# Optimization experiments

Measured on AMD Instinct MI355X. Metric: run time of the kernel, lower is better.

## Reference

```python
import jax, jax.numpy as jnp
import numpy as np

APP_DIM = 27
FEA_PE = 6
VIEW_PE = 6
FEATURE_C = 128
DENSITY_SHIFT = -10.0
DISTANCE_SCALE = 25.0
IN_MLPC = 2 * VIEW_PE * 3 + 2 * FEA_PE * APP_DIM + 3 + APP_DIM  # 390


def positional_encoding(x, freqs):
    # x: [..., C] -> [..., 2*freqs*C]
    freq_bands = (2.0 ** jnp.arange(freqs)).astype(x.dtype)
    pts = (x[..., None] * freq_bands).reshape(x.shape[:-1] + (freqs * x.shape[-1],))
    return jnp.concatenate([jnp.sin(pts), jnp.cos(pts)], axis=-1)


def alpha2weights(alpha):
    # alpha: [N_rays, N_samples]; last sample forced opaque (as in source)
    alpha = alpha.at[:, -1].set(1.0)
    trans = jnp.concatenate(
        [jnp.ones((alpha.shape[0], 1), alpha.dtype), 1.0 - alpha + 1e-10], axis=-1)
    T = jnp.cumprod(trans, axis=-1)
    weights = alpha * T[:, :-1]
    return weights, T


def setup_inputs() -> dict:
    key = jax.random.key(0)
    ks = jax.random.split(key, 12)
    N_rays, N_samples = 4096, 128
    sigma_feat = jax.random.normal(ks[0], (N_rays, N_samples), jnp.float32)
    app_features = 0.1 * jax.random.normal(ks[1], (N_rays, N_samples, APP_DIM), jnp.float32)
    vd = jax.random.normal(ks[2], (N_rays, N_samples, 3), jnp.float32)
    viewdirs = vd / (jnp.linalg.norm(vd, axis=-1, keepdims=True) + 1e-8)
    dists = 0.02 * jax.random.uniform(ks[3], (N_rays, N_samples), jnp.float32)

    def linear(k, fan_in, fan_out):
        kw, kb = jax.random.split(k)
        lim = 1.0 / np.sqrt(fan_in)
        W = jax.random.uniform(kw, (fan_in, fan_out), jnp.float32, -lim, lim)
        b = jax.random.uniform(kb, (fan_out,), jnp.float32, -lim, lim)
        return W, b

    W1, b1 = linear(ks[4], IN_MLPC, FEATURE_C)
    W2, b2 = linear(ks[5], FEATURE_C, FEATURE_C)
    W3, _ = linear(ks[6], FEATURE_C, 3)
    b3 = jnp.zeros((3,), jnp.float32)  # bias of last layer initialized to 0 in source
    return {"sigma_feat": sigma_feat, "app_features": app_features,
            "viewdirs": viewdirs, "dists": dists,
            "W1": W1, "b1": b1, "W2": W2, "b2": b2, "W3": W3, "b3": b3}


def reference(sigma_feat, app_features, viewdirs, dists, W1, b1, W2, b2, W3, b3):
    # feature2density: softplus with density_shift
    sigma = jax.nn.softplus(sigma_feat + DENSITY_SHIFT)
    alpha = 1.0 - jnp.exp(-sigma * dists * DISTANCE_SCALE)  # [N_rays, N_samples]
    weights, _T = alpha2weights(alpha)

    # MLPRender_Fea: cat[features, viewdirs, PE(features), PE(viewdirs)]
    mlp_in = jnp.concatenate(
        [app_features, viewdirs,
         positional_encoding(app_features, FEA_PE),
         positional_encoding(viewdirs, VIEW_PE)], axis=-1)  # [R, S, 390]
    h = jax.nn.relu(jnp.einsum('rsc,cf->rsf', mlp_in, W1) + b1)
    h = jax.nn.relu(jnp.einsum('rsf,fg->rsg', h, W2) + b2)
    rgb = jax.nn.sigmoid(jnp.einsum('rsg,go->rso', h, W3) + b3)  # [R, S, 3]

    rgb_map = jnp.sum(weights[..., None] * rgb, axis=-2)  # [R, 3]
    return rgb_map
```

## Files before the change

### kernel.cpp

```cpp
#include <hip/hip_runtime.h>
#include <math.h>

typedef unsigned short u16;
using bf16x8 = __attribute__((ext_vector_type(8))) short;
using f32x4  = __attribute__((ext_vector_type(4))) float;

#define NS      128
#define NBLOCKS 4096
#define KS1     15
#define NSLICE  19

#define POOLSZ 16384

#define BAR() do { asm volatile("s_waitcnt lgkmcnt(0)" ::: "memory");        \
                   __builtin_amdgcn_s_barrier();                              \
                   asm volatile("" ::: "memory"); } while (0)

#define MF(A,B,C) __builtin_amdgcn_mfma_f32_16x16x32_bf16((A),(B),(C),0,0,0)

__device__ __forceinline__ u16 f2bf(float f) {
    unsigned int i = __float_as_uint(f);
    return (u16)((i + 0x7FFFu + ((i >> 16) & 1u)) >> 16);
}

__device__ __forceinline__ unsigned pk(float hi, float lo) {
    unsigned r;
    asm("v_cvt_pk_bf16_f32 %0, %1, %2" : "=v"(r) : "v"(lo), "v"(hi));
    return r;
}
__device__ __forceinline__ u16 f2bf1(float f) {
    return (u16)((__float_as_uint(f) + 0x8000u) >> 16);
}

__device__ __forceinline__ int afoff_h(int m, int k) {
    int chunk = ((k >> 5) * 8 + (m >> 4)) * 64 + ((k >> 3) & 3) * 16 + (m & 15);
    chunk ^= (k >> 3) & 3;
    return chunk * 8 + (k & 7);
}

__device__ __forceinline__ int orig_k(int ch, int slot) {
    if (ch < 27) {
        if (slot == 0) return ch;
        if (slot <= 6) return 30 + ch * 6 + (slot - 1);
        return 192 + ch * 6 + (slot - 7);
    } else {
        int c = ch - 27;
        if (slot == 0) return 27 + c;
        if (slot <= 6) return 354 + c * 6 + (slot - 1);
        return 372 + c * 6 + (slot - 7);
    }
}

__device__ __forceinline__ float ldch(const float* ap, const float* vp, int c) {
    return (c < 27) ? ap[c] : vp[c - 27];
}

__device__ __forceinline__ void build_x(u16* Xb, int m_b, int cl_b, float v) {
    float rev = v * 0.15915494309189535f;
    rev -= floorf(rev);
    float s0 = __builtin_amdgcn_sinf(rev);
    float c0 = __builtin_amdgcn_cosf(rev);
    float s1 = 2.f * s0 * c0, c1 = c0 * c0 - s0 * s0;
    float s2 = 2.f * s1 * c1, c2 = c1 * c1 - s1 * s1;
    float s3 = 2.f * s2 * c2, c3 = c2 * c2 - s2 * s2;
    float s4 = 2.f * s3 * c3, c4 = c3 * c3 - s3 * s3;
    float s5 = 2.f * s4 * c4, c5 = c4 * c4 - s4 * s4;
    uint4 lo, hi;
    lo.x = pk(s0, v);  lo.y = pk(s2, s1);  lo.z = pk(s4, s3);  lo.w = pk(c0, s5);
    hi.x = pk(c2, c1); hi.y = pk(c4, c3);  hi.z = pk(0.f, c5); hi.w = 0u;
    int base = (m_b >> 4) * 512 + ((2 * cl_b) * 16 + (m_b & 15)) * 8;
    *(uint4*)(Xb + base)       = lo;
    *(uint4*)(Xb + base + 128) = hi;
}

__global__ __launch_bounds__(256) void prep_kernel(
    const float* __restrict__ W1, const float* __restrict__ W2,
    const float* __restrict__ W3, u16* __restrict__ ws)
{
    int idx = blockIdx.x * 256 + threadIdx.x;
    if (idx < 61440) {
        int j = idx & 7, lane = (idx >> 3) & 63, nt = (idx >> 9) & 7, ks = idx >> 12;
        int q = lane >> 4, l15 = lane & 15;
        int klocal = q * 8 + j;
        int ch = ks * 2 + (klocal >> 4);
        int slot = klocal & 15;
        int n = nt * 16 + l15;
        ws[idx] = (slot < 13) ? f2bf(W1[orig_k(ch, slot) * 128 + n]) : (u16)0;
    } else if (idx < 77824) {
        int i2 = idx - 61440;
        int j = i2 & 7, lane = (i2 >> 3) & 63, nt = (i2 >> 9) & 7, ks = i2 >> 12;
        int k = ks * 32 + (lane >> 4) * 8 + j;
        int n = nt * 16 + (lane & 15);
        ws[idx] = f2bf(W2[k * 128 + n]);
    } else if (idx < 79872) {
        int i3 = idx - 77824;
        int j = i3 & 7, lane = (i3 >> 3) & 63, ks = i3 >> 9;
        int k = ks * 32 + (lane >> 4) * 8 + j;
        int n = lane & 15;
        ws[idx] = (n < 3) ? f2bf(W3[k * 3 + n]) : (u16)0;
    }
}

#define LOADB(N0,N1,N2,N3, s)                                                 \
    if ((s) < NSLICE) {                                                       \
        const u16* wp = wp0 + (s) * 4096;                                     \
        N0 = *(const bf16x8*)(wp);                                            \
        N1 = *(const bf16x8*)(wp + 512);                                      \
        N2 = *(const bf16x8*)(wp + 1024);                                     \
        N3 = *(const bf16x8*)(wp + 1536);                                     \
    }

#define BODYX(s, C0,C1,C2,C3, N0,N1,N2,N3)                                    \
  {                                                                           \
    LOADB(N0,N1,N2,N3, (s)+2);                                                \
    const u16* ab = pool + ((((s)>>1)&1) ? 8192 : 0) + (((s)&1)*4096)         \
                    + (wm*128 + lane)*8;                                      \
    bf16x8 a0 = *(const bf16x8*)(ab);                                         \
    bf16x8 a1 = *(const bf16x8*)(ab + 512);                                   \
    __builtin_amdgcn_s_setprio(1);                                            \
    acc[0][0]=MF(a0,C0,acc[0][0]); acc[0][1]=MF(a0,C1,acc[0][1]);             \
    acc[0][2]=MF(a0,C2,acc[0][2]); acc[0][3]=MF(a0,C3,acc[0][3]);             \
    acc[1][0]=MF(a1,C0,acc[1][0]); acc[1][1]=MF(a1,C1,acc[1][1]);             \
    acc[1][2]=MF(a1,C2,acc[1][2]); acc[1][3]=MF(a1,C3,acc[1][3]);             \
    __builtin_amdgcn_s_setprio(0);                                            \
  }

#define BODYH(s, C0,C1,C2,C3, N0,N1,N2,N3)                                    \
  {                                                                           \
    LOADB(N0,N1,N2,N3, (s)+2);                                                \
    int cb0 = ((((s)-15)*512) + wm*128 + lane) ^ quad;                        \
    bf16x8 a0 = *(const bf16x8*)(pool + cb0*8);                               \
    bf16x8 a1 = *(const bf16x8*)(pool + (cb0+64)*8);                          \
    __builtin_amdgcn_s_setprio(1);                                            \
    acc[0][0]=MF(a0,C0,acc[0][0]); acc[0][1]=MF(a0,C1,acc[0][1]);             \
    acc[0][2]=MF(a0,C2,acc[0][2]); acc[0][3]=MF(a0,C3,acc[0][3]);             \
    acc[1][0]=MF(a1,C0,acc[1][0]); acc[1][1]=MF(a1,C1,acc[1][1]);             \
    acc[1][2]=MF(a1,C2,acc[1][2]); acc[1][3]=MF(a1,C3,acc[1][3]);             \
    __builtin_amdgcn_s_setprio(0);                                            \
  }

#define GEND(g)                                                               \
  {                                                                           \
    if (4*((g)+3) + cl < 30) pv_nxt2 = ldch(ap, vp, 4*((g)+3) + cl);          \
    if (4*((g)+1) + cl < 30)                                                  \
        build_x(pool + ((((g)+1)&1) ? 8192 : 0) + (cl>>1)*4096, row, cl&1,    \
                pv_cur);                                                      \
    pv_cur = pv_nxt; pv_nxt = pv_nxt2;                                        \
    BAR();                                                                    \
  }

__global__ __launch_bounds__(512, 4) void render_kernel(
    const float* __restrict__ sigma_g, const float* __restrict__ app_g,
    const float* __restrict__ view_g,  const float* __restrict__ dists_g,
    const float* __restrict__ b1_g,    const float* __restrict__ b2_g,
    const float* __restrict__ b3_g,    const u16* __restrict__ ws,
    float* __restrict__ out_g)
{
    __shared__ __align__(16) u16 pool[POOLSZ];
    __shared__ __align__(16) float part[NS * 3];
    __shared__ float scanS;
    __shared__ float sum2[6];

    const int tid  = threadIdx.x;
    const int lane = tid & 63;
    const int wave = tid >> 6;
    const int l15  = lane & 15;
    const int quad = lane >> 4;
    const int wm   = wave >> 1;
    const int wn   = wave & 1;

    const int r  = blockIdx.x;
    const int rb = r * NS;
    const int row = tid & 127;
    const int cl  = tid >> 7;
    const float* ap = app_g  + (rb + row) * 27;
    const float* vp = view_g + (rb + row) * 3;

    const u16* wp0 = ws + wn * 2048 + lane * 8;
    bf16x8 bP0, bP1, bP2, bP3, bQ0, bQ1, bQ2, bQ3, bR0, bR1, bR2, bR3;
    LOADB(bP0, bP1, bP2, bP3, 0);
    LOADB(bQ0, bQ1, bQ2, bQ3, 1);

    float b1r[4];
    #pragma unroll
    for (int nt = 0; nt < 4; ++nt) b1r[nt] = b1_g[wn * 64 + nt * 16 + l15];

    float pv_cur  = ldch(ap, vp, cl);
    float pv_nxt  = ldch(ap, vp, 4 + cl);
    float pv_nxt2 = ldch(ap, vp, 8 + cl);

    float alpha = 0.f, prod = 1.f, wr = 0.f;
    if (tid < NS) {
        float x  = sigma_g[rb + tid] - 10.f;
        float sp = (x > 20.f) ? x : log1pf(expf(x));
        alpha = 1.f - expf(-sp * dists_g[rb + tid] * 25.f);
        if (tid == NS - 1) alpha = 1.f;
        float tb = 1.f - alpha + 1e-10f;
        prod = tb;
        #pragma unroll
        for (int d = 1; d < 64; d <<= 1) {
            float v = __shfl_up(prod, d);
            if (lane >= d) prod *= v;
        }
        if (tid == 63) scanS = prod;
    }

    build_x(pool + (cl >> 1) * 4096, row, cl & 1, pv_cur);
    pv_cur = pv_nxt; pv_nxt = pv_nxt2;
    BAR();

    if (tid < NS) {
        float prev = __shfl_up(prod, 1);
        float base = (lane == 0) ? 1.f : prev;
        float scale = (wave == 1) ? scanS : 1.f;
        wr = alpha * base * scale;
    }

    const f32x4 vzero = {0.f, 0.f, 0.f, 0.f};
    f32x4 acc[2][4];
    #pragma unroll
    for (int mt = 0; mt < 2; ++mt)
        #pragma unroll
        for (int nt = 0; nt < 4; ++nt) acc[mt][nt] = vzero;

    BODYX(0,  bP0,bP1,bP2,bP3, bR0,bR1,bR2,bR3);
    BODYX(1,  bQ0,bQ1,bQ2,bQ3, bP0,bP1,bP2,bP3);  GEND(0);
    BODYX(2,  bR0,bR1,bR2,bR3, bQ0,bQ1,bQ2,bQ3);
    BODYX(3,  bP0,bP1,bP2,bP3, bR0,bR1,bR2,bR3);  GEND(1);
    BODYX(4,  bQ0,bQ1,bQ2,bQ3, bP0,bP1,bP2,bP3);
    BODYX(5,  bR0,bR1,bR2,bR3, bQ0,bQ1,bQ2,bQ3);  GEND(2);
    BODYX(6,  bP0,bP1,bP2,bP3, bR0,bR1,bR2,bR3);
    BODYX(7,  bQ0,bQ1,bQ2,bQ3, bP0,bP1,bP2,bP3);  GEND(3);
    BODYX(8,  bR0,bR1,bR2,bR3, bQ0,bQ1,bQ2,bQ3);
    BODYX(9,  bP0,bP1,bP2,bP3, bR0,bR1,bR2,bR3);  GEND(4);
    BODYX(10, bQ0,bQ1,bQ2,bQ3, bP0,bP1,bP2,bP3);
    BODYX(11, bR0,bR1,bR2,bR3, bQ0,bQ1,bQ2,bQ3);  GEND(5);
    BODYX(12, bP0,bP1,bP2,bP3, bR0,bR1,bR2,bR3);
    BODYX(13, bQ0,bQ1,bQ2,bQ3, bP0,bP1,bP2,bP3);  GEND(6);
    BODYX(14, bR0,bR1,bR2,bR3, bQ0,bQ1,bQ2,bQ3);
    BAR();

    #pragma unroll
    for (int mt = 0; mt < 2; ++mt)
        #pragma unroll
        for (int nt = 0; nt < 4; ++nt) {
            int col = wn * 64 + nt * 16 + l15;
            #pragma unroll
            for (int rr = 0; rr < 4; ++rr) {
                int rw = wm * 32 + mt * 16 + quad * 4 + rr;
                pool[afoff_h(rw, col)] =
                    f2bf1(fmaxf(acc[mt][nt][rr] + b1r[nt], 0.f));
            }
            acc[mt][nt] = vzero;
        }
    BAR();

    BODYH(15, bP0,bP1,bP2,bP3, bR0,bR1,bR2,bR3);
    BODYH(16, bQ0,bQ1,bQ2,bQ3, bP0,bP1,bP2,bP3);
    BODYH(17, bR0,bR1,bR2,bR3, bQ0,bQ1,bQ2,bQ3);
    BODYH(18, bP0,bP1,bP2,bP3, bR0,bR1,bR2,bR3);
    BAR();

    float b2r[4];
    #pragma unroll
    for (int nt = 0; nt < 4; ++nt) b2r[nt] = b2_g[wn * 64 + nt * 16 + l15];
    #pragma unroll
    for (int mt = 0; mt < 2; ++mt)
        #pragma unroll
        for (int nt = 0; nt < 4; ++nt) {
            int col = wn * 64 + nt * 16 + l15;
            #pragma unroll
            for (int rr = 0; rr < 4; ++rr) {
                int rw = wm * 32 + mt * 16 + quad * 4 + rr;
                pool[afoff_h(rw, col)] =
                    f2bf1(fmaxf(acc[mt][nt][rr] + b2r[nt], 0.f));
            }
        }
    BAR();

    const u16* w3r = ws + 77824;
    const float b3v = (l15 < 3) ? b3_g[l15] : 0.f;
    f32x4 acc3 = vzero;
    #pragma unroll
    for (int ks = 0; ks < 4; ++ks) {
        bf16x8 w3f = *(const bf16x8*)(w3r + (ks * 64 + lane) * 8);
        int c = ((ks * 8 + wave) * 64 + lane) ^ quad;
        bf16x8 a3 = *(const bf16x8*)(pool + c * 8);
        acc3 = MF(a3, w3f, acc3);
    }
    if (l15 < 3) {
        #pragma unroll
        for (int rr = 0; rr < 4; ++rr) {
            int rw = wave * 16 + quad * 4 + rr;
            float v = acc3[rr] + b3v;
            part[rw * 3 + l15] = 1.f / (1.f + expf(-v));
        }
    }
    BAR();

    if (tid < NS) {
        float v0 = wr * part[tid * 3 + 0];
        float v1 = wr * part[tid * 3 + 1];
        float v2 = wr * part[tid * 3 + 2];
        #pragma unroll
        for (int d = 1; d < 64; d <<= 1) {
            v0 += __shfl_xor(v0, d);
            v1 += __shfl_xor(v1, d);
            v2 += __shfl_xor(v2, d);
        }
        if (lane == 0) {
            sum2[wave * 3 + 0] = v0;
            sum2[wave * 3 + 1] = v1;
            sum2[wave * 3 + 2] = v2;
        }
    }
    BAR();
    if (tid == 0) {
        out_g[r * 3 + 0] = sum2[0] + sum2[3];
        out_g[r * 3 + 1] = sum2[1] + sum2[4];
        out_g[r * 3 + 2] = sum2[2] + sum2[5];
    }
}

extern "C" void kernel_launch(void* const* d_in, const int* in_sizes, int n_in,
                              void* d_out, int out_size, void* d_ws, size_t ws_size,
                              hipStream_t stream) {
    (void)in_sizes; (void)n_in; (void)out_size; (void)ws_size;
    const float* sigma = (const float*)d_in[0];
    const float* app   = (const float*)d_in[1];
    const float* view  = (const float*)d_in[2];
    const float* dists = (const float*)d_in[3];
    const float* W1    = (const float*)d_in[4];
    const float* b1    = (const float*)d_in[5];
    const float* W2    = (const float*)d_in[6];
    const float* b2    = (const float*)d_in[7];
    const float* W3    = (const float*)d_in[8];
    const float* b3    = (const float*)d_in[9];
    float* out = (float*)d_out;

    u16* ws = (u16*)d_ws;

    prep_kernel<<<312, 256, 0, stream>>>(W1, W2, W3, ws);
    render_kernel<<<NBLOCKS, 512, 0, stream>>>(sigma, app, view, dists,
                                               b1, b2, b3, ws, out);
}
```

Before: 217.4 us.

## Split each ray across two 256-thread blocks with atomic output accumulation

```diff
diff --git a/kernel.cpp b/kernel.cpp
--- a/kernel.cpp
+++ b/kernel.cpp
@@ -6,11 +6,11 @@
 using f32x4  = __attribute__((ext_vector_type(4))) float;
 
 #define NS      128
-#define NBLOCKS 4096
+#define NBLOCKS 8192
 #define KS1     15
 #define NSLICE  19
 
-#define POOLSZ 16384
+#define POOLSZ 8192
 
 #define BAR() do { asm volatile("s_waitcnt lgkmcnt(0)" ::: "memory");        \
                    __builtin_amdgcn_s_barrier();                              \
@@ -33,9 +33,9 @@
 }
 
 __device__ __forceinline__ int afoff_h(int m, int k) {
-    int chunk = ((k >> 5) * 8 + (m >> 4)) * 64 + ((k >> 3) & 3) * 16 + (m & 15);
+    int chunk = (m >> 4) * 64 + ((k >> 3) & 3) * 16 + (m & 15);
     chunk ^= (k >> 3) & 3;
-    return chunk * 8 + (k & 7);
+    return (k >> 5) * 2048 + chunk * 8 + (k & 7);
 }
 
 __device__ __forceinline__ int orig_k(int ch, int slot) {
@@ -55,7 +55,7 @@
     return (c < 27) ? ap[c] : vp[c - 27];
 }
 
-__device__ __forceinline__ void build_x(u16* Xb, int m_b, int cl_b, float v) {
+__device__ __forceinline__ void build_x(u16* dst, float v) {
     float rev = v * 0.15915494309189535f;
     rev -= floorf(rev);
     float s0 = __builtin_amdgcn_sinf(rev);
@@ -68,16 +68,17 @@
     uint4 lo, hi;
     lo.x = pk(s0, v);  lo.y = pk(s2, s1);  lo.z = pk(s4, s3);  lo.w = pk(c0, s5);
     hi.x = pk(c2, c1); hi.y = pk(c4, c3);  hi.z = pk(0.f, c5); hi.w = 0u;
-    int base = (m_b >> 4) * 512 + ((2 * cl_b) * 16 + (m_b & 15)) * 8;
-    *(uint4*)(Xb + base)       = lo;
-    *(uint4*)(Xb + base + 128) = hi;
+    *(uint4*)(dst)       = lo;
+    *(uint4*)(dst + 128) = hi;
 }
 
 __global__ __launch_bounds__(256) void prep_kernel(
     const float* __restrict__ W1, const float* __restrict__ W2,
-    const float* __restrict__ W3, u16* __restrict__ ws)
+    const float* __restrict__ W3, u16* __restrict__ ws,
+    float* __restrict__ out)
 {
     int idx = blockIdx.x * 256 + threadIdx.x;
+    if (idx < 12288) out[idx] = 0.f;
     if (idx < 61440) {
         int j = idx & 7, lane = (idx >> 3) & 63, nt = (idx >> 9) & 7, ks = idx >> 12;
         int q = lane >> 4, l15 = lane & 15;
@@ -101,7 +102,7 @@
     }
 }
 
-#define LOADB(N0,N1,N2,N3, s)                                                 \
+#define LOADB4(N0,N1,N2,N3, s)                                                \
     if ((s) < NSLICE) {                                                       \
         const u16* wp = wp0 + (s) * 4096;                                     \
         N0 = *(const bf16x8*)(wp);                                            \
@@ -112,8 +113,8 @@
 
 #define BODYX(s, C0,C1,C2,C3, N0,N1,N2,N3)                                    \
   {                                                                           \
-    LOADB(N0,N1,N2,N3, (s)+2);                                                \
-    const u16* ab = pool + ((((s)>>1)&1) ? 8192 : 0) + (((s)&1)*4096)         \
+    LOADB4(N0,N1,N2,N3, (s)+1);                                               \
+    const u16* ab = pool + ((((s)>>1)&1) ? 4096 : 0) + (((s)&1)*2048)         \
                     + (wm*128 + lane)*8;                                      \
     bf16x8 a0 = *(const bf16x8*)(ab);                                         \
     bf16x8 a1 = *(const bf16x8*)(ab + 512);                                   \
@@ -127,10 +128,10 @@
 
 #define BODYH(s, C0,C1,C2,C3, N0,N1,N2,N3)                                    \
   {                                                                           \
-    LOADB(N0,N1,N2,N3, (s)+2);                                                \
-    int cb0 = ((((s)-15)*512) + wm*128 + lane) ^ quad;                        \
-    bf16x8 a0 = *(const bf16x8*)(pool + cb0*8);                               \
-    bf16x8 a1 = *(const bf16x8*)(pool + (cb0+64)*8);                          \
+    LOADB4(N0,N1,N2,N3, (s)+1);                                               \
+    int cb = (((s)-15)*256);                                                  \
+    bf16x8 a0 = *(const bf16x8*)(pool + (cb + ((wm*128 + lane) ^ quad))*8);   \
+    bf16x8 a1 = *(const bf16x8*)(pool + (cb + ((wm*128 + 64 + lane) ^ quad))*8);\
     __builtin_amdgcn_s_setprio(1);                                            \
     acc[0][0]=MF(a0,C0,acc[0][0]); acc[0][1]=MF(a0,C1,acc[0][1]);             \
     acc[0][2]=MF(a0,C2,acc[0][2]); acc[0][3]=MF(a0,C3,acc[0][3]);             \
@@ -141,15 +142,15 @@
 
 #define GEND(g)                                                               \
   {                                                                           \
-    if (4*((g)+3) + cl < 30) pv_nxt2 = ldch(ap, vp, 4*((g)+3) + cl);          \
     if (4*((g)+1) + cl < 30)                                                  \
-        build_x(pool + ((((g)+1)&1) ? 8192 : 0) + (cl>>1)*4096, row, cl&1,    \
+        build_x(pool + ((((g)+1)&1) ? 4096 : 0) + (cl>>1)*2048 + bxoff,       \
                 pv_cur);                                                      \
-    pv_cur = pv_nxt; pv_nxt = pv_nxt2;                                        \
+    pv_cur = pv_nxt;                                                          \
+    if (4*((g)+3) + cl < 30) pv_nxt = ldch(ap, vp, 4*((g)+3) + cl);           \
     BAR();                                                                    \
   }
 
-__global__ __launch_bounds__(512, 4) void render_kernel(
+__global__ __launch_bounds__(256, 5) void render_kernel(
     const float* __restrict__ sigma_g, const float* __restrict__ app_g,
     const float* __restrict__ view_g,  const float* __restrict__ dists_g,
     const float* __restrict__ b1_g,    const float* __restrict__ b2_g,
@@ -157,9 +158,8 @@
     float* __restrict__ out_g)
 {
     __shared__ __align__(16) u16 pool[POOLSZ];
-    __shared__ __align__(16) float part[NS * 3];
+    __shared__ __align__(16) float part[64 * 3];
     __shared__ float scanS;
-    __shared__ float sum2[6];
 
     const int tid  = threadIdx.x;
     const int lane = tid & 63;
@@ -169,25 +169,21 @@
     const int wm   = wave >> 1;
     const int wn   = wave & 1;
 
-    const int r  = blockIdx.x;
-    const int rb = r * NS;
-    const int row = tid & 127;
-    const int cl  = tid >> 7;
-    const float* ap = app_g  + (rb + row) * 27;
-    const float* vp = view_g + (rb + row) * 3;
-
-    const u16* wp0 = ws + wn * 2048 + lane * 8;
-    bf16x8 bP0, bP1, bP2, bP3, bQ0, bQ1, bQ2, bQ3, bR0, bR1, bR2, bR3;
-    LOADB(bP0, bP1, bP2, bP3, 0);
-    LOADB(bQ0, bQ1, bQ2, bQ3, 1);
-
-    float b1r[4];
-    #pragma unroll
-    for (int nt = 0; nt < 4; ++nt) b1r[nt] = b1_g[wn * 64 + nt * 16 + l15];
-
-    float pv_cur  = ldch(ap, vp, cl);
-    float pv_nxt  = ldch(ap, vp, 4 + cl);
-    float pv_nxt2 = ldch(ap, vp, 8 + cl);
+    const int r    = blockIdx.x >> 1;
+    const int half = blockIdx.x & 1;
+    const int rb   = r * NS;
+    const int row  = tid & 63;
+    const int cl   = tid >> 6;
+    const float* ap = app_g  + (rb + half * 64 + row) * 27;
+    const float* vp = view_g + (rb + half * 64 + row) * 3;
+    const int bxoff = (row >> 4) * 512 + (((cl & 1) * 32) + (row & 15)) * 8;
+
+    const u16* wp0 = ws + (wn * 256 + lane) * 8;
+    bf16x8 bP0, bP1, bP2, bP3, bQ0, bQ1, bQ2, bQ3;
+    LOADB4(bP0, bP1, bP2, bP3, 0);
+
+    float pv_cur = ldch(ap, vp, cl);
+    float pv_nxt = ldch(ap, vp, 4 + cl);
 
     float alpha = 0.f, prod = 1.f, wr = 0.f;
     if (tid < NS) {
@@ -205,8 +201,9 @@
         if (tid == 63) scanS = prod;
     }
 
-    build_x(pool + (cl >> 1) * 4096, row, cl & 1, pv_cur);
-    pv_cur = pv_nxt; pv_nxt = pv_nxt2;
+    build_x(pool + (cl >> 1) * 2048 + bxoff, pv_cur);
+    pv_cur = pv_nxt;
+    pv_nxt = ldch(ap, vp, 8 + cl);
     BAR();
 
     if (tid < NS) {
@@ -223,21 +220,24 @@
         #pragma unroll
         for (int nt = 0; nt < 4; ++nt) acc[mt][nt] = vzero;
 
-    BODYX(0,  bP0,bP1,bP2,bP3, bR0,bR1,bR2,bR3);
+    BODYX(0,  bP0,bP1,bP2,bP3, bQ0,bQ1,bQ2,bQ3);
     BODYX(1,  bQ0,bQ1,bQ2,bQ3, bP0,bP1,bP2,bP3);  GEND(0);
-    BODYX(2,  bR0,bR1,bR2,bR3, bQ0,bQ1,bQ2,bQ3);
-    BODYX(3,  bP0,bP1,bP2,bP3, bR0,bR1,bR2,bR3);  GEND(1);
-    BODYX(4,  bQ0,bQ1,bQ2,bQ3, bP0,bP1,bP2,bP3);
-    BODYX(5,  bR0,bR1,bR2,bR3, bQ0,bQ1,bQ2,bQ3);  GEND(2);
-    BODYX(6,  bP0,bP1,bP2,bP3, bR0,bR1,bR2,bR3);
+    BODYX(2,  bP0,bP1,bP2,bP3, bQ0,bQ1,bQ2,bQ3);
+    BODYX(3,  bQ0,bQ1,bQ2,bQ3, bP0,bP1,bP2,bP3);  GEND(1);
+    BODYX(4,  bP0,bP1,bP2,bP3, bQ0,bQ1,bQ2,bQ3);
+    BODYX(5,  bQ0,bQ1,bQ2,bQ3, bP0,bP1,bP2,bP3);  GEND(2);
+    BODYX(6,  bP0,bP1,bP2,bP3, bQ0,bQ1,bQ2,bQ3);
     BODYX(7,  bQ0,bQ1,bQ2,bQ3, bP0,bP1,bP2,bP3);  GEND(3);
-    BODYX(8,  bR0,bR1,bR2,bR3, bQ0,bQ1,bQ2,bQ3);
-    BODYX(9,  bP0,bP1,bP2,bP3, bR0,bR1,bR2,bR3);  GEND(4);
-    BODYX(10, bQ0,bQ1,bQ2,bQ3, bP0,bP1,bP2,bP3);
-    BODYX(11, bR0,bR1,bR2,bR3, bQ0,bQ1,bQ2,bQ3);  GEND(5);
-    BODYX(12, bP0,bP1,bP2,bP3, bR0,bR1,bR2,bR3);
+    BODYX(8,  bP0,bP1,bP2,bP3, bQ0,bQ1,bQ2,bQ3);
+    BODYX(9,  bQ0,bQ1,bQ2,bQ3, bP0,bP1,bP2,bP3);  GEND(4);
+    BODYX(10, bP0,bP1,bP2,bP3, bQ0,bQ1,bQ2,bQ3);
+    BODYX(11, bQ0,bQ1,bQ2,bQ3, bP0,bP1,bP2,bP3);  GEND(5);
+    BODYX(12, bP0,bP1,bP2,bP3, bQ0,bQ1,bQ2,bQ3);
     BODYX(13, bQ0,bQ1,bQ2,bQ3, bP0,bP1,bP2,bP3);  GEND(6);
-    BODYX(14, bR0,bR1,bR2,bR3, bQ0,bQ1,bQ2,bQ3);
+    BODYX(14, bP0,bP1,bP2,bP3, bQ0,bQ1,bQ2,bQ3);
+    float b1r[4];
+    #pragma unroll
+    for (int nt = 0; nt < 4; ++nt) b1r[nt] = b1_g[wn * 64 + nt * 16 + l15];
     BAR();
 
     #pragma unroll
@@ -255,10 +255,10 @@
         }
     BAR();
 
-    BODYH(15, bP0,bP1,bP2,bP3, bR0,bR1,bR2,bR3);
-    BODYH(16, bQ0,bQ1,bQ2,bQ3, bP0,bP1,bP2,bP3);
-    BODYH(17, bR0,bR1,bR2,bR3, bQ0,bQ1,bQ2,bQ3);
-    BODYH(18, bP0,bP1,bP2,bP3, bR0,bR1,bR2,bR3);
+    BODYH(15, bQ0,bQ1,bQ2,bQ3, bP0,bP1,bP2,bP3);
+    BODYH(16, bP0,bP1,bP2,bP3, bQ0,bQ1,bQ2,bQ3);
+    BODYH(17, bQ0,bQ1,bQ2,bQ3, bP0,bP1,bP2,bP3);
+    BODYH(18, bP0,bP1,bP2,bP3, bQ0,bQ1,bQ2,bQ3);
     BAR();
 
     float b2r[4];
@@ -284,7 +284,7 @@
     #pragma unroll
     for (int ks = 0; ks < 4; ++ks) {
         bf16x8 w3f = *(const bf16x8*)(w3r + (ks * 64 + lane) * 8);
-        int c = ((ks * 8 + wave) * 64 + lane) ^ quad;
+        int c = ks * 256 + ((wave * 64 + lane) ^ quad);
         bf16x8 a3 = *(const bf16x8*)(pool + c * 8);
         acc3 = MF(a3, w3f, acc3);
     }
@@ -298,10 +298,11 @@
     }
     BAR();
 
-    if (tid < NS) {
-        float v0 = wr * part[tid * 3 + 0];
-        float v1 = wr * part[tid * 3 + 1];
-        float v2 = wr * part[tid * 3 + 2];
+    if ((tid >> 6) == half) {
+        int local = tid & 63;
+        float v0 = wr * part[local * 3 + 0];
+        float v1 = wr * part[local * 3 + 1];
+        float v2 = wr * part[local * 3 + 2];
         #pragma unroll
         for (int d = 1; d < 64; d <<= 1) {
             v0 += __shfl_xor(v0, d);
@@ -309,16 +310,10 @@
             v2 += __shfl_xor(v2, d);
         }
         if (lane == 0) {
-            sum2[wave * 3 + 0] = v0;
-            sum2[wave * 3 + 1] = v1;
-            sum2[wave * 3 + 2] = v2;
-        }
-    }
-    BAR();
-    if (tid == 0) {
-        out_g[r * 3 + 0] = sum2[0] + sum2[3];
-        out_g[r * 3 + 1] = sum2[1] + sum2[4];
-        out_g[r * 3 + 2] = sum2[2] + sum2[5];
+            atomicAdd(&out_g[r * 3 + 0], v0);
+            atomicAdd(&out_g[r * 3 + 1], v1);
+            atomicAdd(&out_g[r * 3 + 2], v2);
+        }
     }
 }
 
@@ -340,7 +335,7 @@
 
     u16* ws = (u16*)d_ws;
 
-    prep_kernel<<<312, 256, 0, stream>>>(W1, W2, W3, ws);
-    render_kernel<<<NBLOCKS, 512, 0, stream>>>(sigma, app, view, dists,
+    prep_kernel<<<312, 256, 0, stream>>>(W1, W2, W3, ws, out);
+    render_kernel<<<NBLOCKS, 256, 0, stream>>>(sigma, app, view, dists,
                                                b1, b2, b3, ws, out);
 }
```

Result: slower. 248.8 us (+14.4%).
